# Kernel tuning notes

Hardware: AMD Instinct MI355X
Metric: run time of the kernel (lower is better)

Reference implementation:

```python
import jax, jax.numpy as jnp
import numpy as np

B, C, H, W = 4, 512, 64, 64
CH = C // 2  # 256


def setup_inputs() -> dict:
    key = jax.random.key(0)
    ks = jax.random.split(key, 10)
    s = 0.02  # keep logits in sane range for softmax
    return {
        "Fc": jax.random.normal(ks[0], (B, C, H, W), jnp.float32),
        "Fs": jax.random.normal(ks[1], (B, C, H, W), jnp.float32),
        "f_w": jax.random.normal(ks[2], (CH, C), jnp.float32) * s,
        "f_b": jax.random.normal(ks[3], (CH,), jnp.float32) * s,
        "g_w": jax.random.normal(ks[4], (CH, C), jnp.float32) * s,
        "g_b": jax.random.normal(ks[5], (CH,), jnp.float32) * s,
        "h_w": jax.random.normal(ks[6], (C, C), jnp.float32) * s,
        "h_b": jax.random.normal(ks[7], (C,), jnp.float32) * s,
        "out_w": jax.random.normal(ks[8], (C, C), jnp.float32) * s,
        "out_b": jax.random.normal(ks[9], (C,), jnp.float32) * s,
    }


def _conv1x1(x, w, b):
    # x: [B,C,H,W], w: [O,C], b: [O] -> [B,O,H,W]
    return jnp.einsum('oc,bchw->bohw', w, x) + b[None, :, None, None]


def reference(Fc, Fs, f_w, f_b, g_w, g_b, h_w, h_b, out_w, out_b):
    b, c, h, w = Fc.shape
    hw = h * w
    Ff = _conv1x1(Fc, f_w, f_b).reshape(b, -1, hw)   # [B, C/2, HW]
    Fg = _conv1x1(Fs, g_w, g_b).reshape(b, -1, hw)   # [B, C/2, HW]
    Fh = _conv1x1(Fs, h_w, h_b).reshape(b, -1, hw)   # [B, C,   HW]
    d_k = Ff.shape[1]  # channels//2, matches torch d_k after permute
    # Attention[b,i,j] over style positions j
    logits = jnp.einsum('bci,bcj->bij', Ff, Fg) / jnp.sqrt(jnp.float32(d_k))
    attn = jax.nn.softmax(logits, axis=-1)           # [B, HW, HW]
    # Out[b,c,i] = sum_j Fh[b,c,j] * attn[b,i,j]
    out = jnp.einsum('bcj,bij->bci', Fh, attn).reshape(b, c, h, w)
    return _conv1x1(out, out_w, out_b) + Fc
```

## Files before the change

### kernel.cpp

```cpp
#include <hip/hip_runtime.h>
#include <hip/hip_bf16.h>

#define HW    4096
#define CDIM  512
#define CHALF 256
#define NB    4
#define FLASH_LDS 132096
#define MERGE_LDS 66048

using bf16 = __hip_bfloat16;
typedef __attribute__((ext_vector_type(8))) short short8;
typedef __attribute__((ext_vector_type(4))) float float4v;

typedef __attribute__((address_space(1))) void gvoid_t;
typedef __attribute__((address_space(3))) void svoid_t;
#define GLD16(gp, lp) \
    __builtin_amdgcn_global_load_lds((gvoid_t*)(gp), (svoid_t*)(lp), 16, 0, 0)
#define MFMA(a, b, c) __builtin_amdgcn_mfma_f32_16x16x32_bf16(a, b, c, 0, 0, 0)

static __device__ __forceinline__ short8 ld_short8(const bf16* p) {
    return *reinterpret_cast<const short8*>(p);
}
static __device__ __forceinline__ float b2f(short s) {
    unsigned u = ((unsigned)(unsigned short)s) << 16;
    return __builtin_bit_cast(float, u);
}
static __device__ __forceinline__ short f2bs(float f) {
    bf16 h = __float2bfloat16(f);
    return __builtin_bit_cast(short, h);
}

__global__ void transpose_cast(const float* __restrict__ Fc,
                               const float* __restrict__ Fs,
                               bf16* __restrict__ FcT, bf16* __restrict__ FsT) {
    __shared__ float tile[32][33];
    int p0 = blockIdx.x * 32, c0 = blockIdx.y * 32;
    int z = blockIdx.z;
    int b = z & 3, which = z >> 2;
    const float* src = (which ? Fs : Fc) + (size_t)b * CDIM * HW;
    bf16* dst = (which ? FsT : FcT) + (size_t)b * HW * CDIM;
    int tx = threadIdx.x, ty = threadIdx.y;
    for (int i = 0; i < 4; i++)
        tile[ty + 8 * i][tx] = src[(size_t)(c0 + ty + 8 * i) * HW + p0 + tx];
    __syncthreads();
    for (int i = 0; i < 4; i++)
        dst[(size_t)(p0 + ty + 8 * i) * CDIM + c0 + tx] =
            __float2bfloat16(tile[tx][ty + 8 * i]);
}

__global__ void cast4(const float* __restrict__ fw, const float* __restrict__ gw,
                      const float* __restrict__ hw, const float* __restrict__ ow,
                      bf16* __restrict__ dst) {
    int i = blockIdx.x * 256 + threadIdx.x;
    float v;
    if (i < 131072)       v = fw[i] * 0.0625f;
    else if (i < 262144)  v = gw[i - 131072];
    else if (i < 524288)  v = hw[i - 262144];
    else                  v = ow[i - 524288];
    dst[i] = __float2bfloat16(v);
}

__launch_bounds__(256, 2)
__global__ void gemm_fg(const bf16* __restrict__ A1, const bf16* __restrict__ A2,
                        size_t sA,
                        const bf16* __restrict__ W1, const bf16* __restrict__ W2,
                        const float* __restrict__ b1, const float* __restrict__ b2,
                        float bs1, float bs2,
                        bf16* __restrict__ D1, bf16* __restrict__ D2, size_t sD,
                        int zhalf, int N, int K) {
    __shared__ bf16 Asf[2][8192];
    __shared__ bf16 Bsf[2][8192];
    int lid = blockIdx.x;
    int xcd = lid & 7, idx = lid >> 3;
    int bx = idx & 1;
    int yzg = xcd * 32 + (idx >> 1);
    int z = yzg >> 5;
    int by = yzg & 31;
    const bf16 *A, *W; const float* bias; float bsc; bf16* D;
    if (z < zhalf) { A = A1 + sA * z;           W = W1; bias = b1; bsc = bs1; D = D1 + sD * z; }
    else           { A = A2 + sA * (z - zhalf); W = W2; bias = b2; bsc = bs2; D = D2 + sD * (z - zhalf); }
    int m0 = by * 128, n0 = bx * 128;
    int t = threadIdx.x;
    int w = t >> 6, lane = t & 63;
    int wm = w >> 1, wn = w & 1;
    int l15 = lane & 15, quad = lane >> 4;
    int lr = lane >> 3, lc = (lane & 7) ^ lr;
    int nk = K >> 6;
    float4v acc[4][4] = {};

    for (int q = 0; q < 4; q++) {
        int rb = w * 32 + q * 8;
        GLD16(A + (size_t)(m0 + rb + lr) * K + lc * 8, &Asf[0][rb * 64]);
        GLD16(W + (size_t)(n0 + rb + lr) * K + lc * 8, &Bsf[0][rb * 64]);
    }
    for (int i = 0; i < nk; i++) {
        __syncthreads();
        if (i + 1 < nk) {
            int k0 = (i + 1) << 6, nb = (i + 1) & 1;
            for (int q = 0; q < 4; q++) {
                int rb = w * 32 + q * 8;
                GLD16(A + (size_t)(m0 + rb + lr) * K + k0 + lc * 8, &Asf[nb][rb * 64]);
                GLD16(W + (size_t)(n0 + rb + lr) * K + k0 + lc * 8, &Bsf[nb][rb * 64]);
            }
        }
        int cb = i & 1;
        for (int h = 0; h < 2; h++) {
            int p = (h * 4 + quad) ^ (l15 & 7);
            short8 af[4], bfr[4];
            for (int sm = 0; sm < 4; sm++)
                af[sm] = *(const short8*)&Asf[cb][(wm * 64 + sm * 16 + l15) * 64 + p * 8];
            for (int sn = 0; sn < 4; sn++)
                bfr[sn] = *(const short8*)&Bsf[cb][(wn * 64 + sn * 16 + l15) * 64 + p * 8];
            for (int sm = 0; sm < 4; sm++)
                for (int sn = 0; sn < 4; sn++)
                    acc[sm][sn] = MFMA(af[sm], bfr[sn], acc[sm][sn]);
        }
    }
    for (int sm = 0; sm < 4; sm++)
        for (int sn = 0; sn < 4; sn++) {
            int n = n0 + wn * 64 + sn * 16 + l15;
            for (int r = 0; r < 4; r++) {
                int m = m0 + wm * 64 + sm * 16 + quad * 4 + r;
                D[(size_t)m * N + n] = __float2bfloat16(acc[sm][sn][r] + bias[n] * bsc);
            }
        }
}

__launch_bounds__(256, 2)
__global__ void gemm_bw(const bf16* __restrict__ Aw,
                        const bf16* __restrict__ Bact, size_t sB,
                        const float* __restrict__ bias,
                        bf16* __restrict__ Dp, size_t sD,
                        int N, int K) {
    __shared__ bf16 Asf[2][8192];
    __shared__ bf16 Bsf[2][8192];
    int lid = blockIdx.x;
    int xcd = lid & 7, idx = lid >> 3;
    int my = idx & 3;
    int nzg = xcd * 16 + (idx >> 2);
    int z = nzg >> 5;
    int nx = nzg & 31;
    const bf16* A = Aw;
    const bf16* Bm = Bact + sB * z;
    int m0 = my * 128, n0 = nx * 128;
    int t = threadIdx.x;
    int w = t >> 6, lane = t & 63;
    int wm = w >> 1, wn = w & 1;
    int l15 = lane & 15, quad = lane >> 4;
    int lr = lane >> 3, lc = (lane & 7) ^ lr;
    int nk = K >> 6;
    float4v acc[4][4] = {};

    for (int q = 0; q < 4; q++) {
        int rb = w * 32 + q * 8;
        GLD16(A + (size_t)(m0 + rb + lr) * K + lc * 8, &Asf[0][rb * 64]);
        GLD16(Bm + (size_t)(n0 + rb + lr) * K + lc * 8, &Bsf[0][rb * 64]);
    }
    for (int i = 0; i < nk; i++) {
        __syncthreads();
        if (i + 1 < nk) {
            int k0 = (i + 1) << 6, nb = (i + 1) & 1;
            for (int q = 0; q < 4; q++) {
                int rb = w * 32 + q * 8;
                GLD16(A + (size_t)(m0 + rb + lr) * K + k0 + lc * 8, &Asf[nb][rb * 64]);
                GLD16(Bm + (size_t)(n0 + rb + lr) * K + k0 + lc * 8, &Bsf[nb][rb * 64]);
            }
        }
        int cb = i & 1;
        for (int h = 0; h < 2; h++) {
            int p = (h * 4 + quad) ^ (l15 & 7);
            short8 af[4], bfr[4];
            for (int sm = 0; sm < 4; sm++)
                af[sm] = *(const short8*)&Asf[cb][(wm * 64 + sm * 16 + l15) * 64 + p * 8];
            for (int sn = 0; sn < 4; sn++)
                bfr[sn] = *(const short8*)&Bsf[cb][(wn * 64 + sn * 16 + l15) * 64 + p * 8];
            for (int sm = 0; sm < 4; sm++)
                for (int sn = 0; sn < 4; sn++)
                    acc[sm][sn] = MFMA(af[sm], bfr[sn], acc[sm][sn]);
        }
    }
    for (int sm = 0; sm < 4; sm++)
        for (int sn = 0; sn < 4; sn++) {
            int n = n0 + wn * 64 + sn * 16 + l15;
            for (int r = 0; r < 4; r++) {
                int m = m0 + wm * 64 + sm * 16 + quad * 4 + r;
                Dp[sD * z + (size_t)m * N + n] =
                    __float2bfloat16(acc[sm][sn][r] + bias[m]);
            }
        }
}

__launch_bounds__(1024)
__global__ void flash_attn(const bf16* __restrict__ Q_, const bf16* __restrict__ Kt_,
                           const bf16* __restrict__ V_,
                           bf16* __restrict__ O0_, bf16* __restrict__ O1_,
                           float* __restrict__ L0_, float* __restrict__ L1_) {
    extern __shared__ char smem[];
    bf16* Qs  = (bf16*)smem;
    bf16* Ksf = (bf16*)(smem + 65536);
    short* Ps = (short*)(smem + 98304);
    float* lpart = (float*)(smem + 131072);

    int lid = blockIdx.x;
    int stream = lid & 7;
    int b = stream & 3, jh = stream >> 2;
    int i0 = (lid >> 3) * 128;
    const bf16* Kt = Kt_ + (size_t)b * HW * CHALF;
    const bf16* V  = V_ + (size_t)b * CDIM * HW;
    bf16* Out   = (jh ? O1_ : O0_) + ((size_t)b * HW + i0) * CDIM;
    float* Lout = (jh ? L1_ : L0_) + (size_t)b * HW + i0;

    int t = threadIdx.x;
    int w = t >> 6, lane = t & 63;
    int l15 = lane & 15, quad = lane >> 4;
    int rg  = w & 7;
    int cg  = w >> 3;
    int ih  = w >> 3;
    int c0w = (w & 7) * 64;
    int jbeg = jh * (HW / 2);

    int r0 = lane >> 5, cc = lane & 31;

    for (int i = 0; i < 4; i++) {
        int rp = i * 16 + w;
        int r = 2 * rp + r0;
        int c = cc ^ (r & 7);
        GLD16(Q_ + ((size_t)b * HW + i0 + r) * CHALF + c * 8, &Qs[rp * 512]);
    }
    for (int i = 0; i < 2; i++) {
        int rp = i * 16 + w;
        int r = 2 * rp + r0;
        int c = cc ^ (r & 7);
        GLD16(Kt + (size_t)(jbeg + r) * CHALF + c * 8, &Ksf[rp * 512]);
    }
    float l_lane[4] = {};
    float4v oacc[4][4] = {};
    asm volatile("s_waitcnt vmcnt(0)" ::: "memory");
    __builtin_amdgcn_s_barrier();

    const bf16* vp = V + (size_t)(c0w + l15) * HW + quad * 8;

    auto qksm = [&](int pb) {
        float4v s0 = {}, s1 = {};
        __builtin_amdgcn_s_setprio(1);
        #pragma unroll
        for (int k8 = 0; k8 < 8; k8++) {
            int pq = ((k8 * 4 + quad) ^ (l15 & 7)) * 8;
            short8 qf = *(const short8*)&Qs[(rg * 16 + l15) * 256 + pq];
            short8 k0 = *(const short8*)&Ksf[(cg * 32 + l15) * 256 + pq];
            short8 k1 = *(const short8*)&Ksf[(cg * 32 + 16 + l15) * 256 + pq];
            s0 = MFMA(qf, k0, s0);
            s1 = MFMA(qf, k1, s1);
        }
        __builtin_amdgcn_s_setprio(0);
        short* Pb = Ps + pb * 8192;
        int cw = cg * 4 + (l15 >> 3);
        #pragma unroll
        for (int r = 0; r < 4; r++) {
            int rl = rg * 16 + quad * 4 + r;
            float p0 = __expf(s0[r]);
            float p1 = __expf(s1[r]);
            l_lane[r] += p0 + p1;
            Pb[rl * 64 + ((cw + rl) & 7) * 8 + (l15 & 7)]     = f2bs(p0);
            Pb[rl * 64 + ((cw + 2 + rl) & 7) * 8 + (l15 & 7)] = f2bs(p1);
        }
    };
    auto pvhalf = [&](int pb, int h, int j0) {
        short8 va[4];
        #pragma unroll
        for (int sn = 0; sn < 4; sn++)
            va[sn] = ld_short8(vp + j0 + h * 32 + (size_t)(sn * 16) * HW);
        __builtin_amdgcn_s_setprio(1);
        #pragma unroll
        for (int sm = 0; sm < 4; sm++) {
            int rl = ih * 64 + sm * 16 + l15;
            short8 pf = *(const short8*)&Ps[pb * 8192 + rl * 64 +
                                            ((h * 4 + quad + rl) & 7) * 8];
            #pragma unroll
            for (int sn = 0; sn < 4; sn++)
                oacc[sm][sn] = MFMA(pf, va[sn], oacc[sm][sn]);
        }
        __builtin_amdgcn_s_setprio(0);
    };

    qksm(0);
    asm volatile("s_waitcnt lgkmcnt(0)" ::: "memory");
    __builtin_amdgcn_s_barrier();

    for (int it = 1; it < 32; it++) {
        int jp = jbeg + (it - 1) * 64;
        for (int i = 0; i < 2; i++) {
            int rp = i * 16 + w;
            int r = 2 * rp + r0;
            int c = cc ^ (r & 7);
            GLD16(Kt + (size_t)(jbeg + it * 64 + r) * CHALF + c * 8,
                  &Ksf[rp * 512]);
        }
        int pb = (it - 1) & 1;
        pvhalf(pb, 0, jp);
        pvhalf(pb, 1, jp);
        asm volatile("s_waitcnt vmcnt(0)" ::: "memory");
        qksm(it & 1);
        asm volatile("s_waitcnt lgkmcnt(0)" ::: "memory");
        __builtin_amdgcn_s_barrier();
    }
    {
        int jp = jbeg + 31 * 64;
        pvhalf(1, 0, jp);
        pvhalf(1, 1, jp);
    }

    #pragma unroll
    for (int r = 0; r < 4; r++) {
        float red = l_lane[r];
        red += __shfl_xor(red, 1);
        red += __shfl_xor(red, 2);
        red += __shfl_xor(red, 4);
        red += __shfl_xor(red, 8);
        if (l15 == 0)
            lpart[cg * 128 + rg * 16 + quad * 4 + r] = red;
    }
    __syncthreads();
    if (t < 128)
        Lout[t] = lpart[t] + lpart[128 + t];
    for (int sm = 0; sm < 4; sm++)
        for (int r = 0; r < 4; r++) {
            int rl = ih * 64 + sm * 16 + quad * 4 + r;
            float li = 1.0f / (lpart[rl] + lpart[128 + rl]);
            for (int sn = 0; sn < 4; sn++)
                Out[(size_t)rl * CDIM + c0w + sn * 16 + l15] =
                    __float2bfloat16(oacc[sm][sn][r] * li);
        }
}

__launch_bounds__(256, 1)
__global__ void merge_out(const bf16* __restrict__ Op0, const bf16* __restrict__ Op1,
                          const float* __restrict__ L0, const float* __restrict__ L1,
                          const bf16* __restrict__ ow, const float* __restrict__ out_b,
                          const float* __restrict__ Fc, float* __restrict__ out) {
    extern __shared__ char smem[];
    short* Os = (short*)smem;
    float* lw = (float*)(smem + 65536);

    int rt = blockIdx.x;
    int b = rt >> 6;
    int i0 = (rt & 63) * 64;
    size_t obase = ((size_t)b * HW + i0) * CDIM;
    int t = threadIdx.x;

    if (t < 64) {
        float l0 = L0[(size_t)b * HW + i0 + t];
        float l1 = L1[(size_t)b * HW + i0 + t];
        float inv = 1.f / (l0 + l1);
        lw[t * 2] = l0 * inv;
        lw[t * 2 + 1] = l1 * inv;
    }
    __syncthreads();

    for (int q = 0; q < 16; q++) {
        int idx = q * 256 + t;
        int row = idx >> 6, cc = idx & 63;
        short8 a = ld_short8(Op0 + obase + (size_t)row * CDIM + cc * 8);
        short8 c = ld_short8(Op1 + obase + (size_t)row * CDIM + cc * 8);
        float w0 = lw[row * 2], w1 = lw[row * 2 + 1];
        short8 o;
        #pragma unroll
        for (int j = 0; j < 8; j++)
            o[j] = f2bs(w0 * b2f(a[j]) + w1 * b2f(c[j]));
        *(short8*)&Os[row * 512 + (cc ^ (row & 7)) * 8] = o;
    }
    __syncthreads();

    int w = t >> 6, lane = t & 63;
    int l15 = lane & 15, quad = lane >> 4;
    int m0 = w * 128;
    float4v acc[8][4] = {};
    for (int k8 = 0; k8 < 16; k8++) {
        short8 bfr[4];
        #pragma unroll
        for (int n16 = 0; n16 < 4; n16++)
            bfr[n16] = *(const short8*)&Os[(n16 * 16 + l15) * 512 +
                (((k8 * 4 + quad) ^ (l15 & 7))) * 8];
        short8 af[8];
        #pragma unroll
        for (int m16 = 0; m16 < 8; m16++)
            af[m16] = ld_short8(ow + (size_t)(m0 + m16 * 16 + l15) * CDIM +
                                k8 * 32 + quad * 8);
        #pragma unroll
        for (int m16 = 0; m16 < 8; m16++)
            for (int n16 = 0; n16 < 4; n16++)
                acc[m16][n16] = MFMA(af[m16], bfr[n16], acc[m16][n16]);
    }

    const float* fcb = Fc + (size_t)b * CDIM * HW;
    float* outb = out + (size_t)b * CDIM * HW;
    for (int m16 = 0; m16 < 8; m16++)
        for (int r = 0; r < 4; r++) {
            int co = m0 + m16 * 16 + quad * 4 + r;
            float bb = out_b[co];
            for (int n16 = 0; n16 < 4; n16++) {
                int i = i0 + n16 * 16 + l15;
                outb[(size_t)co * HW + i] =
                    acc[m16][n16][r] + bb + fcb[(size_t)co * HW + i];
            }
        }
}

extern "C" void kernel_launch(void* const* d_in, const int* in_sizes, int n_in,
                              void* d_out, int out_size, void* d_ws, size_t ws_size,
                              hipStream_t stream) {
    const float* Fc   = (const float*)d_in[0];
    const float* Fs   = (const float*)d_in[1];
    const float* f_w  = (const float*)d_in[2];
    const float* f_b  = (const float*)d_in[3];
    const float* g_w  = (const float*)d_in[4];
    const float* g_b  = (const float*)d_in[5];
    const float* h_w  = (const float*)d_in[6];
    const float* h_b  = (const float*)d_in[7];
    const float* out_w = (const float*)d_in[8];
    const float* out_b = (const float*)d_in[9];
    float* out = (float*)d_out;

    bf16* FcT = (bf16*)d_ws;
    bf16* FsT = FcT + (size_t)NB * HW * CDIM;
    bf16* FfT = FsT + (size_t)NB * HW * CDIM;
    bf16* FgT = FfT + (size_t)NB * HW * CHALF;
    bf16* Fh  = FgT + (size_t)NB * HW * CHALF;
    bf16* fw  = Fh  + (size_t)NB * CDIM * HW;
    bf16* gw  = fw + (size_t)CHALF * CDIM;
    bf16* hw  = gw + (size_t)CHALF * CDIM;
    bf16* ow  = hw + (size_t)CDIM * CDIM;
    float* L0 = (float*)(ow + (size_t)CDIM * CDIM);
    float* L1 = L0 + (size_t)NB * HW;
    bf16* Op0 = FcT;
    bf16* Op1 = FsT;

    hipFuncSetAttribute((const void*)flash_attn,
                        hipFuncAttributeMaxDynamicSharedMemorySize, FLASH_LDS);
    hipFuncSetAttribute((const void*)merge_out,
                        hipFuncAttributeMaxDynamicSharedMemorySize, MERGE_LDS);

    transpose_cast<<<dim3(HW / 32, CDIM / 32, NB * 2), dim3(32, 8), 0, stream>>>(
        Fc, Fs, FcT, FsT);
    cast4<<<dim3(786432 / 256), 256, 0, stream>>>(f_w, g_w, h_w, out_w, fw);

    gemm_fg<<<dim3(512), 256, 0, stream>>>(
        FcT, FsT, (size_t)HW * CDIM, fw, gw, f_b, g_b, 0.0625f, 1.0f,
        FfT, FgT, (size_t)HW * CHALF, NB, CHALF, CDIM);
    gemm_bw<<<dim3(512), 256, 0, stream>>>(
        hw, FsT, (size_t)HW * CDIM, h_b, Fh, (size_t)CDIM * HW, HW, CDIM);
    flash_attn<<<dim3(256), 1024, FLASH_LDS, stream>>>(
        FfT, FgT, Fh, Op0, Op1, L0, L1);
    merge_out<<<dim3(256), 256, MERGE_LDS, stream>>>(
        Op0, Op1, L0, L1, ow, out_b, Fc, out);
}
```

Measured before the change: 401.6 us.

## Double KV tile to 128 and drop P double-buffering in flash attention

The flash attention kernel now processes 128 key positions per iteration instead of 64, so there are half as many loop iterations. The QK^T stage uses 2x2 MFMA register tiles per wave, and the P buffer becomes a single 128-wide buffer. To stay correct with one P buffer, the loop adds an extra barrier between PV and the next QK/softmax, which removes the earlier overlap of PV with the next QK step. LDS use grows to 160KB; the row-sum scratch reuses the Q region, which is safe only after the final barrier.

```diff
diff --git a/kernel.cpp b/kernel.cpp
--- a/kernel.cpp
+++ b/kernel.cpp
@@ -5,7 +5,7 @@
 #define CDIM  512
 #define CHALF 256
 #define NB    4
-#define FLASH_LDS 132096
+#define FLASH_LDS 163840
 #define MERGE_LDS 66048
 
 using bf16 = __hip_bfloat16;
@@ -198,8 +198,8 @@
     extern __shared__ char smem[];
     bf16* Qs  = (bf16*)smem;
     bf16* Ksf = (bf16*)(smem + 65536);
-    short* Ps = (short*)(smem + 98304);
-    float* lpart = (float*)(smem + 131072);
+    short* Ps = (short*)(smem + 131072);
+    float* lpart = (float*)smem;
 
     int lid = blockIdx.x;
     int stream = lid & 7;
@@ -213,122 +213,132 @@
     int t = threadIdx.x;
     int w = t >> 6, lane = t & 63;
     int l15 = lane & 15, quad = lane >> 4;
-    int rg  = w & 7;
-    int cg  = w >> 3;
-    int ih  = w >> 3;
-    int c0w = (w & 7) * 64;
+    int rq = w & 3,  cq = w >> 2;
+    int rv = w >> 3, cv = w & 7;
     int jbeg = jh * (HW / 2);
-
     int r0 = lane >> 5, cc = lane & 31;
 
     for (int i = 0; i < 4; i++) {
-        int rp = i * 16 + w;
-        int r = 2 * rp + r0;
+        int sup = i * 16 + w;
+        int r = 2 * sup + r0;
         int c = cc ^ (r & 7);
-        GLD16(Q_ + ((size_t)b * HW + i0 + r) * CHALF + c * 8, &Qs[rp * 512]);
-    }
-    for (int i = 0; i < 2; i++) {
-        int rp = i * 16 + w;
-        int r = 2 * rp + r0;
+        GLD16(Q_ + ((size_t)b * HW + i0 + r) * CHALF + c * 8, &Qs[sup * 512]);
+    }
+    for (int i = 0; i < 4; i++) {
+        int sup = i * 16 + w;
+        int r = 2 * sup + r0;
         int c = cc ^ (r & 7);
-        GLD16(Kt + (size_t)(jbeg + r) * CHALF + c * 8, &Ksf[rp * 512]);
-    }
-    float l_lane[4] = {};
+        GLD16(Kt + (size_t)(jbeg + r) * CHALF + c * 8, &Ksf[sup * 512]);
+    }
+    float l_lane[2][4] = {};
     float4v oacc[4][4] = {};
     asm volatile("s_waitcnt vmcnt(0)" ::: "memory");
     __builtin_amdgcn_s_barrier();
 
-    const bf16* vp = V + (size_t)(c0w + l15) * HW + quad * 8;
-
-    auto qksm = [&](int pb) {
-        float4v s0 = {}, s1 = {};
+    const bf16* vp = V + (size_t)(cv * 64 + l15) * HW + quad * 8;
+
+    auto qksm = [&]() {
+        float4v s00 = {}, s01 = {}, s10 = {}, s11 = {};
         __builtin_amdgcn_s_setprio(1);
         #pragma unroll
-        for (int k8 = 0; k8 < 8; k8++) {
-            int pq = ((k8 * 4 + quad) ^ (l15 & 7)) * 8;
-            short8 qf = *(const short8*)&Qs[(rg * 16 + l15) * 256 + pq];
-            short8 k0 = *(const short8*)&Ksf[(cg * 32 + l15) * 256 + pq];
-            short8 k1 = *(const short8*)&Ksf[(cg * 32 + 16 + l15) * 256 + pq];
-            s0 = MFMA(qf, k0, s0);
-            s1 = MFMA(qf, k1, s1);
+        for (int ks = 0; ks < 8; ks++) {
+            int pq = ((ks * 4 + quad) ^ (l15 & 7)) * 8;
+            short8 a0 = *(const short8*)&Qs[(rq * 32 + l15) * 256 + pq];
+            short8 a1 = *(const short8*)&Qs[(rq * 32 + 16 + l15) * 256 + pq];
+            short8 b0 = *(const short8*)&Ksf[(cq * 32 + l15) * 256 + pq];
+            short8 b1 = *(const short8*)&Ksf[(cq * 32 + 16 + l15) * 256 + pq];
+            s00 = MFMA(a0, b0, s00);
+            s01 = MFMA(a0, b1, s01);
+            s10 = MFMA(a1, b0, s10);
+            s11 = MFMA(a1, b1, s11);
         }
         __builtin_amdgcn_s_setprio(0);
-        short* Pb = Ps + pb * 8192;
-        int cw = cg * 4 + (l15 >> 3);
+        int gj0 = cq * 4 + (l15 >> 3);
+        int gj1 = gj0 + 2;
         #pragma unroll
         for (int r = 0; r < 4; r++) {
-            int rl = rg * 16 + quad * 4 + r;
-            float p0 = __expf(s0[r]);
-            float p1 = __expf(s1[r]);
-            l_lane[r] += p0 + p1;
-            Pb[rl * 64 + ((cw + rl) & 7) * 8 + (l15 & 7)]     = f2bs(p0);
-            Pb[rl * 64 + ((cw + 2 + rl) & 7) * 8 + (l15 & 7)] = f2bs(p1);
+            int rl0 = rq * 32 + quad * 4 + r, rl1 = rl0 + 16;
+            float p00 = __expf(s00[r]);
+            float p01 = __expf(s01[r]);
+            float p10 = __expf(s10[r]);
+            float p11 = __expf(s11[r]);
+            l_lane[0][r] += p00 + p01;
+            l_lane[1][r] += p10 + p11;
+            Ps[rl0 * 128 + ((gj0 + rl0) & 15) * 8 + (l15 & 7)] = f2bs(p00);
+            Ps[rl0 * 128 + ((gj1 + rl0) & 15) * 8 + (l15 & 7)] = f2bs(p01);
+            Ps[rl1 * 128 + ((gj0 + rl1) & 15) * 8 + (l15 & 7)] = f2bs(p10);
+            Ps[rl1 * 128 + ((gj1 + rl1) & 15) * 8 + (l15 & 7)] = f2bs(p11);
         }
     };
-    auto pvhalf = [&](int pb, int h, int j0) {
-        short8 va[4];
-        #pragma unroll
-        for (int sn = 0; sn < 4; sn++)
-            va[sn] = ld_short8(vp + j0 + h * 32 + (size_t)(sn * 16) * HW);
+    auto pv = [&](int jp) {
         __builtin_amdgcn_s_setprio(1);
         #pragma unroll
-        for (int sm = 0; sm < 4; sm++) {
-            int rl = ih * 64 + sm * 16 + l15;
-            short8 pf = *(const short8*)&Ps[pb * 8192 + rl * 64 +
-                                            ((h * 4 + quad + rl) & 7) * 8];
+        for (int ks = 0; ks < 4; ks++) {
+            short8 vf[4];
             #pragma unroll
             for (int sn = 0; sn < 4; sn++)
-                oacc[sm][sn] = MFMA(pf, va[sn], oacc[sm][sn]);
+                vf[sn] = ld_short8(vp + jp + ks * 32 + (size_t)(sn * 16) * HW);
+            short8 pf[4];
+            #pragma unroll
+            for (int sm = 0; sm < 4; sm++) {
+                int rl = rv * 64 + sm * 16 + l15;
+                pf[sm] = *(const short8*)&Ps[rl * 128 +
+                                             (((ks * 4 + quad) + rl) & 15) * 8];
+            }
+            #pragma unroll
+            for (int sm = 0; sm < 4; sm++)
+                #pragma unroll
+                for (int sn = 0; sn < 4; sn++)
+                    oacc[sm][sn] = MFMA(pf[sm], vf[sn], oacc[sm][sn]);
         }
         __builtin_amdgcn_s_setprio(0);
     };
 
-    qksm(0);
+    qksm();
     asm volatile("s_waitcnt lgkmcnt(0)" ::: "memory");
     __builtin_amdgcn_s_barrier();
 
-    for (int it = 1; it < 32; it++) {
-        int jp = jbeg + (it - 1) * 64;
-        for (int i = 0; i < 2; i++) {
-            int rp = i * 16 + w;
-            int r = 2 * rp + r0;
+    for (int it = 1; it < 16; it++) {
+        for (int i = 0; i < 4; i++) {
+            int sup = i * 16 + w;
+            int r = 2 * sup + r0;
             int c = cc ^ (r & 7);
-            GLD16(Kt + (size_t)(jbeg + it * 64 + r) * CHALF + c * 8,
-                  &Ksf[rp * 512]);
-        }
-        int pb = (it - 1) & 1;
-        pvhalf(pb, 0, jp);
-        pvhalf(pb, 1, jp);
-        asm volatile("s_waitcnt vmcnt(0)" ::: "memory");
-        qksm(it & 1);
+            GLD16(Kt + (size_t)(jbeg + it * 128 + r) * CHALF + c * 8,
+                  &Ksf[sup * 512]);
+        }
+        pv(jbeg + (it - 1) * 128);
         asm volatile("s_waitcnt lgkmcnt(0)" ::: "memory");
         __builtin_amdgcn_s_barrier();
-    }
-    {
-        int jp = jbeg + 31 * 64;
-        pvhalf(1, 0, jp);
-        pvhalf(1, 1, jp);
-    }
+        asm volatile("s_waitcnt vmcnt(0)" ::: "memory");
+        qksm();
+        asm volatile("s_waitcnt lgkmcnt(0)" ::: "memory");
+        __builtin_amdgcn_s_barrier();
+    }
+    pv(jbeg + 15 * 128);
+    __builtin_amdgcn_s_barrier();
 
     #pragma unroll
-    for (int r = 0; r < 4; r++) {
-        float red = l_lane[r];
-        red += __shfl_xor(red, 1);
-        red += __shfl_xor(red, 2);
-        red += __shfl_xor(red, 4);
-        red += __shfl_xor(red, 8);
-        if (l15 == 0)
-            lpart[cg * 128 + rg * 16 + quad * 4 + r] = red;
-    }
+    for (int h = 0; h < 2; h++)
+        #pragma unroll
+        for (int r = 0; r < 4; r++) {
+            float red = l_lane[h][r];
+            red += __shfl_xor(red, 1);
+            red += __shfl_xor(red, 2);
+            red += __shfl_xor(red, 4);
+            red += __shfl_xor(red, 8);
+            if (l15 == 0)
+                lpart[cq * 128 + rq * 32 + h * 16 + quad * 4 + r] = red;
+        }
     __syncthreads();
     if (t < 128)
-        Lout[t] = lpart[t] + lpart[128 + t];
+        Lout[t] = lpart[t] + lpart[128 + t] + lpart[256 + t] + lpart[384 + t];
     for (int sm = 0; sm < 4; sm++)
         for (int r = 0; r < 4; r++) {
-            int rl = ih * 64 + sm * 16 + quad * 4 + r;
-            float li = 1.0f / (lpart[rl] + lpart[128 + rl]);
+            int rl = rv * 64 + sm * 16 + quad * 4 + r;
+            float li = 1.0f / (lpart[rl] + lpart[128 + rl] +
+                               lpart[256 + rl] + lpart[384 + rl]);
             for (int sn = 0; sn < 4; sn++)
-                Out[(size_t)rl * CDIM + c0w + sn * 16 + l15] =
+                Out[(size_t)rl * CDIM + cv * 64 + sn * 16 + l15] =
                     __float2bfloat16(oacc[sm][sn][r] * li);
         }
 }
```

Measured after the change: 473.3 us. 1.18x slower.
